# Kernel tuning notes

Measured on AMD Instinct MI355X. Metric: run time of the kernel, lower is better.

Reference implementation:

```python
import jax, jax.numpy as jnp
import numpy as np
from jax import lax

L = 5; HID = 100; B = 4; H = 256; W = 256; MU = 0.02; SLOPE = 0.01

def conv2d(x, w, pad=1, groups=1):
    return lax.conv_general_dilated(x, w, (1, 1), ((pad, pad), (pad, pad)),
                                    dimension_numbers=('NCHW', 'OIHW', 'NCHW'),
                                    feature_group_count=groups)

def leaky(x):
    return jnp.where(x >= 0, x, SLOPE * x)

def res_block(x, w1, w2, w3):
    # dropout omitted (eval-mode reference)
    h = leaky(conv2d(x, w1))
    h = leaky(conv2d(h, w2))
    return conv2d(h, w3)

def gauss1d(size=51, sigma=10.0):
    x = jnp.arange(size, dtype=jnp.float32) - (size - 1) / 2.0
    g = jnp.exp(-0.5 * (x / sigma) ** 2)
    return g / g.sum()

def gaussian_blur(x):
    # kornia GaussianBlur2d((51,51),(10,10), border 'constant') == zero-pad separable blur
    C = x.shape[1]
    g = gauss1d()
    kh = jnp.tile(g.reshape(1, 1, 1, 51), (C, 1, 1, 1))
    kv = jnp.tile(g.reshape(1, 1, 51, 1), (C, 1, 1, 1))
    x = lax.conv_general_dilated(x, kh, (1, 1), ((0, 0), (25, 25)),
                                 dimension_numbers=('NCHW', 'OIHW', 'NCHW'), feature_group_count=C)
    x = lax.conv_general_dilated(x, kv, (1, 1), ((25, 25), (0, 0)),
                                 dimension_numbers=('NCHW', 'OIHW', 'NCHW'), feature_group_count=C)
    return x

def spatial_gradient(x):
    # kornia SpatialGradient('sobel', normalized): kernels /8, replicate padding -> [B,C,2,H,W]
    Bk, C, Hk, Wk = x.shape
    kx = jnp.array([[-1., 0., 1.], [-2., 0., 2.], [-1., 0., 1.]], dtype=x.dtype) / 8.0
    k = jnp.stack([kx, kx.T])[:, None]          # [2,1,3,3]
    k = jnp.tile(k, (C, 1, 1, 1))               # [2C,1,3,3]
    xp = jnp.pad(x, ((0, 0), (0, 0), (1, 1), (1, 1)), mode='edge')
    out = conv2d(xp, k, pad=0, groups=C)        # [B,2C,H,W]
    return out.reshape(Bk, C, 2, Hk, Wk)

def deform_image(img, grid):
    # img [B,C,H,W]; grid [B,2,H,W] pixel coords (x,y); bilinear grid_sample, zeros outside
    Bk, C, Hk, Wk = img.shape
    x, y = grid[:, 0], grid[:, 1]
    x0 = jnp.floor(x); y0 = jnp.floor(y)
    wx1 = x - x0; wy1 = y - y0
    flat = img.reshape(Bk, C, Hk * Wk)
    def tap(xi, yi, wgt):
        valid = (xi >= 0) & (xi <= Wk - 1) & (yi >= 0) & (yi <= Hk - 1)
        xc = jnp.clip(xi, 0, Wk - 1).astype(jnp.int32)
        yc = jnp.clip(yi, 0, Hk - 1).astype(jnp.int32)
        idx = (yc * Wk + xc).reshape(Bk, 1, Hk * Wk)
        v = jnp.take_along_axis(flat, idx, axis=2).reshape(Bk, C, Hk, Wk)
        return v * (wgt * valid.astype(img.dtype))[:, None]
    return (tap(x0, y0, (1 - wx1) * (1 - wy1)) + tap(x0 + 1, y0, wx1 * (1 - wy1))
            + tap(x0, y0 + 1, (1 - wx1) * wy1) + tap(x0 + 1, y0 + 1, wx1 * wy1))

def forward(source, source_seg, z0, zw1, zw2, zw3, vw1, vw2, vw3):
    Bk, _, Hk, Wk = source.shape
    l = zw1.shape[0]
    yy, xx = jnp.meshgrid(jnp.arange(Hk, dtype=source.dtype), jnp.arange(Wk, dtype=source.dtype), indexing='ij')
    deformation = jnp.broadcast_to(jnp.stack([xx, yy])[None], (Bk, 2, Hk, Wk))  # pixel-coord id grid
    images = [source]
    residuals = [jnp.broadcast_to(z0, (Bk,) + z0.shape[1:])]
    residuals_deformed = [residuals[0]]
    fields = []
    grads = [spatial_gradient(source)]
    for i in range(l):
        zin = jnp.concatenate([residuals[i], images[i], images[0]], axis=1)  # 3 channels
        f = res_block(zin, zw1[i], zw2[i], zw3[i]) / l
        residuals.append(residuals[i] + f)
        residuals_deformed = [deform_image(z, deformation) for z in residuals_deformed]
        residuals_deformed.append(residuals[-1])
        vin = jnp.concatenate([deformation, images[-1]], axis=1)  # 3 channels
        fields.append(gaussian_blur(res_block(vin, vw1[i], vw2[i], vw3[i])))
        deformation = deformation - fields[i] / l
        mask = deform_image(source_seg, deformation)
        acc = residuals_deformed[1]
        for z in residuals_deformed[2:]:
            acc = acc + z
        new_img = deform_image(images[0], deformation) + acc * (MU ** 2 / l) * mask
        images.append(new_img)
        grads.append(spatial_gradient(new_img))
    return jnp.stack(images), jnp.stack(fields), jnp.stack(residuals), jnp.stack(grads)

def setup_inputs() -> dict:
    key = jax.random.key(0)
    ks = jax.random.split(key, 9)
    def rn(k, shape, s):
        return s * jax.random.normal(k, shape, dtype=jnp.float32)
    return {
        'source': rn(ks[0], (B, 1, H, W), 1.0),
        'source_seg': jax.random.uniform(ks[1], (B, 1, H, W), dtype=jnp.float32),
        'z0': rn(ks[2], (1, 1, H, W), 0.05),
        'zw1': rn(ks[3], (L, HID, 3, 3, 3), 0.2),
        'zw2': rn(ks[4], (L, HID, HID, 3, 3), 0.033),
        'zw3': rn(ks[5], (L, 1, HID, 3, 3), 0.033),
        'vw1': rn(ks[6], (L, HID, 3, 3, 3), 0.02),
        'vw2': rn(ks[7], (L, HID, HID, 3, 3), 0.033),
        'vw3': rn(ks[8], (L, 2, HID, 3, 3), 0.033),
    }

def reference(source, source_seg, z0, zw1, zw2, zw3, vw1, vw2, vw3):
    return forward(source, source_seg, z0, zw1, zw2, zw3, vw1, vw2, vw3)
```

## Files before the change

### kernel.cpp

```cpp
#include <hip/hip_runtime.h>
#include <math.h>

#define HW 65536
#define BB 4
#define NL 5

typedef short s8v __attribute__((ext_vector_type(8)));
typedef float f4v __attribute__((ext_vector_type(4)));
typedef unsigned short u16;

#define AS1 __attribute__((address_space(1)))
#define AS3 __attribute__((address_space(3)))

__device__ __forceinline__ float leaky_f(float x){ return x >= 0.f ? x : 0.01f * x; }

__device__ __forceinline__ u16 f2bf(float x){
    union { float f; unsigned u; } v; v.f = x;
    unsigned r = v.u + 0x7FFF + ((v.u >> 16) & 1);
    return (u16)(r >> 16);
}
__device__ __forceinline__ float bf2f(u16 h){
    union { unsigned u; float f; } v; v.u = ((unsigned)h) << 16;
    return v.f;
}

__global__ void k_init(const float* __restrict__ src, const float* __restrict__ z0,
                       float* __restrict__ images0, float* __restrict__ resid0,
                       float* __restrict__ def){
    int p = blockIdx.x * 256 + threadIdx.x;
    int b = p >> 16, q = p & 65535;
    images0[p] = src[p];
    resid0[p]  = z0[q];
    int x = q & 255, y = q >> 8;
    def[(size_t)(b * 2 + 0) * HW + q] = (float)x;
    def[(size_t)(b * 2 + 1) * HW + q] = (float)y;
}

__global__ void k_grad(const float* __restrict__ img, float* __restrict__ gout){
    int p = blockIdx.x * 256 + threadIdx.x;
    int b = p >> 16, q = p & 65535;
    int x = q & 255, y = q >> 8;
    const float* ib = img + (size_t)b * HW;
    int xm = max(x - 1, 0), xp = min(x + 1, 255);
    int ym = max(y - 1, 0), yp = min(y + 1, 255);
    float a00 = ib[ym * 256 + xm], a01 = ib[ym * 256 + x], a02 = ib[ym * 256 + xp];
    float a10 = ib[y  * 256 + xm],                         a12 = ib[y  * 256 + xp];
    float a20 = ib[yp * 256 + xm], a21 = ib[yp * 256 + x], a22 = ib[yp * 256 + xp];
    float gx = (a02 - a00 + 2.f * (a12 - a10) + a22 - a20) * 0.125f;
    float gy = (a20 - a00 + 2.f * (a21 - a01) + a22 - a02) * 0.125f;
    gout[(size_t)(b * 2 + 0) * HW + q] = gx;
    gout[(size_t)(b * 2 + 1) * HW + q] = gy;
}

__global__ void k_packw(const float* __restrict__ zw2, const float* __restrict__ vw2,
                        u16* __restrict__ wp){
    int idx = blockIdx.x * 256 + threadIdx.x;
    int lane9 = idx & 511, chunk = idx >> 9;
    int nt = chunk & 7; int t = chunk >> 3;
    int ks = t % 4; t >>= 2;
    int off = t % 9; t /= 9;
    int layer = t % 5, path = t / 5;
    int lane = lane9 >> 3, j = lane9 & 7;
    int ic = ks * 32 + (lane >> 4) * 8 + j;
    int oc = nt * 16 + (lane & 15);
    const float* w = path ? vw2 : zw2;
    float v = 0.f;
    if (ic < 100 && oc < 100)
        v = w[(((size_t)layer * 100 + oc) * 100 + ic) * 9 + off];
    wp[idx] = f2bf(v);
}

__global__ void k_packw3(const float* __restrict__ zw3, const float* __restrict__ vw3,
                         u16* __restrict__ wq){
    int idx = blockIdx.x * 256 + threadIdx.x;
    if (idx >= 184320) return;
    int lane9 = idx & 511, chunk = idx >> 9;
    int ks = chunk & 3; int t = chunk >> 2;
    int off = t % 9; int slot = t / 9;
    int lane = lane9 >> 3, j = lane9 & 7;
    int ic = ks * 32 + (lane >> 4) * 8 + j;
    int oc = lane & 15;
    float v = 0.f;
    if (ic < 100){
        if (slot < 5){ if (oc == 0) v = zw3[((size_t)slot * 100 + ic) * 9 + off]; }
        else { int layer = slot - 5;
               if (oc < 2) v = vw3[(((size_t)layer * 2 + oc) * 100 + ic) * 9 + off]; }
    }
    wq[idx] = f2bf(v);
}

__global__ __launch_bounds__(256)
void k_conv1(const float* __restrict__ p0, int s0, const float* __restrict__ p1, int s1,
             const float* __restrict__ p2, int s2, const float* __restrict__ w1,
             u16* __restrict__ h1, int b0){
    __shared__ float t3[300];
    __shared__ float wl[2700];
    const int tid = threadIdx.x;
    const int tX = blockIdx.x, tY = blockIdx.y, bz = blockIdx.z;
    const int b = b0 + bz;
    const int y0 = tY * 8 - 1, x0 = tX * 8 - 1;
    for (int idx = tid; idx < 300; idx += 256){
        int ch = idx / 100, p = idx - ch * 100;
        int r = p / 10, c = p - r * 10;
        int gy = y0 + r, gx = x0 + c;
        const float* pp = (ch == 0) ? p0 + (size_t)b * s0
                        : (ch == 1) ? p1 + (size_t)b * s1 : p2 + (size_t)b * s2;
        t3[idx] = ((unsigned)gy < 256u && (unsigned)gx < 256u) ? pp[gy * 256 + gx] : 0.f;
    }
    for (int idx = tid; idx < 2700; idx += 256) wl[idx] = w1[idx];
    __syncthreads();

    const int px = tid & 63, g = tid >> 6;
    const int row = px >> 3, colx = px & 7;
    float iv[27];
    #pragma unroll
    for (int c3 = 0; c3 < 3; c3++)
        #pragma unroll
        for (int dr = 0; dr < 3; dr++)
            #pragma unroll
            for (int dc = 0; dc < 3; dc++)
                iv[c3 * 9 + dr * 3 + dc] = t3[c3 * 100 + (row + dr) * 10 + colx + dc];

    const int gy = tY * 8 + row, gx = tX * 8 + colx;
    u16* dst = h1 + (((size_t)bz * HW + (size_t)(gy * 256 + gx)) << 7) + g * 32;
    #pragma unroll
    for (int s = 0; s < 4; s++){
        int ov[4];
        #pragma unroll
        for (int hp = 0; hp < 4; hp++){
            u16 lo = 0, hi = 0;
            #pragma unroll
            for (int e = 0; e < 2; e++){
                int oc = g * 32 + s * 8 + hp * 2 + e;
                u16 hv = 0;
                if (oc < 100){
                    const float* wk = &wl[oc * 27];
                    float a = 0.f;
                    #pragma unroll
                    for (int q = 0; q < 27; q++) a = fmaf(wk[q], iv[q], a);
                    hv = f2bf(leaky_f(a));
                }
                if (e) hi = hv; else lo = hv;
            }
            ov[hp] = (int)lo | ((int)hi << 16);
        }
        *(int4*)(dst + s * 8) = make_int4(ov[0], ov[1], ov[2], ov[3]);
    }
}

__device__ __forceinline__ void dma_setup(const u16* __restrict__ h, size_t hbase,
                                          int y0, int x0, int tid,
                                          const u16** gp, int* gstep){
    const u16* zpad = h + (hbase << 7) + 112;
    #pragma unroll
    for (int s = 0; s < 6; s++){
        int idx = tid + s * 256;
        const u16* g = zpad; int st = 0;
        if (idx < 1360){
            int px = idx >> 2, part = idx & 3;
            int hr = px / 34, hc = px - hr * 34;
            int gy = y0 + hr, gx = x0 + hc;
            if ((unsigned)gy < 256u && (unsigned)gx < 256u){
                g = h + ((hbase + (size_t)(gy * 256 + gx)) << 7) + (part ^ ((px >> 1) & 3)) * 8;
                st = 32;
            }
        }
        gp[s] = g; gstep[s] = st;
    }
}

__device__ __forceinline__ void dma_slab(const u16** gp, const int* gstep,
                                         short* Lnxt, int wv){
    #pragma unroll
    for (int s = 0; s < 6; s++){
        __builtin_amdgcn_global_load_lds(
            (const AS1 unsigned int*)(unsigned long long)(const void*)gp[s],
            (AS3 unsigned int*)(unsigned long long)(void*)(&Lnxt[(s * 256 + wv * 64) * 8]),
            16, 0, 0);
        gp[s] += gstep[s];
    }
}

__global__ __launch_bounds__(256, 2)
void k_conv2(const u16* __restrict__ h1, const u16* __restrict__ wp, u16* __restrict__ h2){
    __shared__ __align__(16) short lds[2][12288];
    const int tid = threadIdx.x;
    const int lane = tid & 63, wv = tid >> 6;
    const int quad = lane >> 4, m = lane & 15;
    const int hhalf = wv & 1, vhalf = wv >> 1;
    const int tX = blockIdx.x, tY = blockIdx.y, bz = blockIdx.z;
    const int y0 = tY * 8 - 1, x0 = tX * 32 - 1;
    const size_t hbase = (size_t)bz << 16;

    f4v acc[4][8];
    #pragma unroll
    for (int t = 0; t < 4; t++)
        #pragma unroll
        for (int n = 0; n < 8; n++){
            acc[t][n][0] = 0.f; acc[t][n][1] = 0.f; acc[t][n][2] = 0.f; acc[t][n][3] = 0.f;
        }

    const u16* gp[6]; int gstep[6];
    dma_setup(h1, hbase, y0, x0, tid, gp, gstep);
    dma_slab(gp, gstep, lds[0], wv);

    const u16* wl = wp + lane * 8;
    s8v af[2][4];
    #pragma unroll
    for (int t = 0; t < 4; t++)
        af[0][t] = *(const s8v*)(wl + (size_t)(4 * hhalf + t) * 512);

    for (int ks = 0; ks < 4; ks++){
        __syncthreads();
        const short* L = lds[ks & 1];
        short* Lnxt = lds[(ks + 1) & 1];
        #pragma unroll
        for (int off = 0; off < 9; off++){
            const int kk = ks * 9 + off;
            if (off == 4 && ks < 3) dma_slab(gp, gstep, Lnxt, wv);
            if (kk < 35){
                int nks = (off == 8) ? ks + 1 : ks;
                int noff = (off == 8) ? 0 : off + 1;
                #pragma unroll
                for (int t = 0; t < 4; t++)
                    af[(kk + 1) & 1][t] =
                        *(const s8v*)(wl + (size_t)((noff * 4 + nks) * 8 + 4 * hhalf + t) * 512);
            }
            const int dr = off / 3, dc = off - dr * 3;
            s8v bf[8];
            #pragma unroll
            for (int n = 0; n < 8; n++){
                int hpx = (4 * vhalf + (n >> 1) + dr) * 34 + (n & 1) * 16 + m + dc;
                bf[n] = *(const s8v*)&L[hpx * 32 + ((quad ^ ((hpx >> 1) & 3)) << 3)];
            }
            #pragma unroll
            for (int t = 0; t < 4; t++)
                #pragma unroll
                for (int n = 0; n < 8; n++)
                    acc[t][n] = __builtin_amdgcn_mfma_f32_16x16x32_bf16(
                        af[kk & 1][t], bf[n], acc[t][n], 0, 0, 0);
        }
    }

    #pragma unroll
    for (int n = 0; n < 8; n++){
        int gy = tY * 8 + 4 * vhalf + (n >> 1);
        int gx = tX * 32 + (n & 1) * 16 + m;
        u16* base = h2 + ((hbase + (size_t)(gy * 256 + gx)) << 7) + 64 * hhalf;
        #pragma unroll
        for (int t = 0; t < 4; t++){
            unsigned lo = (unsigned)f2bf(leaky_f(acc[t][n][0])) |
                          ((unsigned)f2bf(leaky_f(acc[t][n][1])) << 16);
            unsigned hi = (unsigned)f2bf(leaky_f(acc[t][n][2])) |
                          ((unsigned)f2bf(leaky_f(acc[t][n][3])) << 16);
            *(int2*)(base + t * 16 + quad * 4) = make_int2((int)lo, (int)hi);
        }
    }
}

template<int N>
__global__ __launch_bounds__(256, 2)
void k_conv3(const u16* __restrict__ h2, const u16* __restrict__ wq,
             const float* __restrict__ rprev, float* __restrict__ out0,
             float* __restrict__ out1, int b0){
    __shared__ __align__(16) short lds[2][12288];
    const int tid = threadIdx.x;
    const int lane = tid & 63, wv = tid >> 6;
    const int quad = lane >> 4, m = lane & 15;
    const int tX = blockIdx.x, tY = blockIdx.y, bz = blockIdx.z;
    const int y0 = tY * 8 - 1, x0 = tX * 32 - 1;
    const size_t hbase = (size_t)bz << 16;

    f4v acc[4];
    #pragma unroll
    for (int t = 0; t < 4; t++){ acc[t][0]=0.f; acc[t][1]=0.f; acc[t][2]=0.f; acc[t][3]=0.f; }

    const u16* gp[6]; int gstep[6];
    dma_setup(h2, hbase, y0, x0, tid, gp, gstep);
    dma_slab(gp, gstep, lds[0], wv);

    for (int ks = 0; ks < 4; ks++){
        __syncthreads();
        const short* L = lds[ks & 1];
        short* Lnxt = lds[(ks + 1) & 1];
        const bool pre = (ks < 3);
        #pragma unroll
        for (int off = 0; off < 9; off++){
            if (off == 4 && pre) dma_slab(gp, gstep, Lnxt, wv);
            const int dr = off / 3, dc = off - dr * 3;
            s8v wf = *(const s8v*)(wq + (size_t)(off * 4 + ks) * 512 + lane * 8);
            #pragma unroll
            for (int t = 0; t < 4; t++){
                int hpx = (2 * wv + (t >> 1) + dr) * 34 + (t & 1) * 16 + dc + m;
                s8v af = *(const s8v*)&L[hpx * 32 + ((quad ^ ((hpx >> 1) & 3)) << 3)];
                acc[t] = __builtin_amdgcn_mfma_f32_16x16x32_bf16(af, wf, acc[t], 0, 0, 0);
            }
        }
    }

    const int b = b0 + bz;
    #pragma unroll
    for (int t = 0; t < 4; t++){
        int gy = tY * 8 + 2 * wv + (t >> 1);
        int gx = tX * 32 + (t & 1) * 16 + quad * 4;
        size_t p = (size_t)gy * 256 + gx;
        if (N == 1){
            if (m == 0){
                float4 rp = *(const float4*)&rprev[(size_t)b * HW + p];
                float4 v = make_float4(rp.x + acc[t][0] * 0.2f, rp.y + acc[t][1] * 0.2f,
                                       rp.z + acc[t][2] * 0.2f, rp.w + acc[t][3] * 0.2f);
                *(float4*)&out0[(size_t)b * HW + p] = v;
                *(float4*)&out1[(size_t)b * HW + p] = v;
            }
        } else {
            if (m < 2){
                float4 v = make_float4(acc[t][0], acc[t][1], acc[t][2], acc[t][3]);
                *(float4*)&out0[((size_t)(b * 2) + m) * HW + p] = v;
            }
        }
    }
}

__device__ __forceinline__ float bilin(const float* __restrict__ img, float x, float y){
    float x0 = floorf(x), y0 = floorf(y);
    float wx = x - x0, wy = y - y0;
    float r = 0.f;
    #pragma unroll
    for (int dy = 0; dy < 2; dy++){
        float yi = y0 + (float)dy;
        if (yi < 0.f || yi > 255.f) continue;
        int iy = (int)yi;
        float wyv = dy ? wy : 1.f - wy;
        #pragma unroll
        for (int dx = 0; dx < 2; dx++){
            float xi = x0 + (float)dx;
            if (xi < 0.f || xi > 255.f) continue;
            int ix = (int)xi;
            float wxv = dx ? wx : 1.f - wx;
            r += wyv * wxv * img[iy * 256 + ix];
        }
    }
    return r;
}

__global__ void k_deform(const float* __restrict__ rdin, const float* __restrict__ def,
                         float* __restrict__ rdout){
    int p = blockIdx.x * 256 + threadIdx.x;
    int j = blockIdx.y;
    int b = p >> 16, q = p & 65535;
    float x = def[(size_t)(b * 2 + 0) * HW + q];
    float y = def[(size_t)(b * 2 + 1) * HW + q];
    rdout[(size_t)j * BB * HW + p] = bilin(rdin + (size_t)j * BB * HW + (size_t)b * HW, x, y);
}

__global__ void k_blur_h(const float* __restrict__ in, float* __restrict__ outb){
    __shared__ float g[51];
    __shared__ float row[306];
    __shared__ float ginv;
    int tid = threadIdx.x;
    int rid = blockIdx.x;
    int ch = rid >> 8, y = rid & 255;
    if (tid < 51){ float d = (float)tid - 25.f; g[tid] = expf(-0.005f * d * d); }
    row[tid + 25] = in[(size_t)ch * HW + y * 256 + tid];
    if (tid < 25) row[tid] = 0.f;
    if (tid >= 231) row[tid + 50] = 0.f;
    __syncthreads();
    if (tid == 0){ float s = 0.f; for (int k = 0; k < 51; k++) s += g[k]; ginv = 1.f / s; }
    __syncthreads();
    float acc = 0.f;
    for (int k = 0; k < 51; k++) acc = fmaf(g[k], row[tid + k], acc);
    outb[(size_t)ch * HW + y * 256 + tid] = acc * ginv;
}

__global__ void k_blur_v(const float* __restrict__ in, float* __restrict__ fout,
                         float* __restrict__ def){
    __shared__ float g[51];
    __shared__ float ginv;
    __shared__ float tb[82 * 64];
    int tid = threadIdx.x;
    int tX = blockIdx.x, tY = blockIdx.y, ch = blockIdx.z;
    if (tid < 51){ float d = (float)tid - 25.f; g[tid] = expf(-0.005f * d * d); }
    for (int idx = tid; idx < 82 * 64; idx += 256){
        int r = idx >> 6, c = idx & 63;
        int gy = tY * 32 + r - 25, gx = tX * 64 + c;
        tb[idx] = (gy >= 0 && gy < 256) ? in[(size_t)ch * HW + gy * 256 + gx] : 0.f;
    }
    __syncthreads();
    if (tid == 0){ float s = 0.f; for (int k = 0; k < 51; k++) s += g[k]; ginv = 1.f / s; }
    __syncthreads();
    int c = tid & 63, r0 = (tid >> 6) * 8;
    for (int k = 0; k < 8; k++){
        int r = r0 + k;
        float acc = 0.f;
        for (int t = 0; t < 51; t++) acc = fmaf(g[t], tb[(r + t) * 64 + c], acc);
        acc *= ginv;
        int y = tY * 32 + r, x = tX * 64 + c;
        fout[(size_t)ch * HW + y * 256 + x] = acc;
        def [(size_t)ch * HW + y * 256 + x] -= acc * 0.2f;
    }
}

__global__ void k_final(const float* __restrict__ def, const float* __restrict__ src,
                        const float* __restrict__ seg, const float* __restrict__ rdbase,
                        int nrd, float* __restrict__ imgout){
    int p = blockIdx.x * 256 + threadIdx.x;
    int b = p >> 16, q = p & 65535;
    float x = def[(size_t)(b * 2 + 0) * HW + q];
    float y = def[(size_t)(b * 2 + 1) * HW + q];
    float mk = bilin(seg + (size_t)b * HW, x, y);
    float s = bilin(src + (size_t)b * HW, x, y);
    float acc = 0.f;
    for (int j = 0; j < nrd; j++) acc += rdbase[(size_t)j * BB * HW + p];
    imgout[p] = s + acc * 8e-5f * mk;
}

extern "C" void kernel_launch(void* const* d_in, const int* in_sizes, int n_in,
                              void* d_out, int out_size, void* d_ws, size_t ws_size,
                              hipStream_t stream){
    const float* source = (const float*)d_in[0];
    const float* seg    = (const float*)d_in[1];
    const float* z0     = (const float*)d_in[2];
    const float* zw1    = (const float*)d_in[3];
    const float* zw2    = (const float*)d_in[4];
    const float* zw3    = (const float*)d_in[5];
    const float* vw1    = (const float*)d_in[6];
    const float* vw2    = (const float*)d_in[7];
    const float* vw3    = (const float*)d_in[8];

    float* out = (float*)d_out;
    float* images = out;
    float* fields = out + 1572864;
    float* resid  = out + 4194304;
    float* grads  = out + 5767168;

    float* ws = (float*)d_ws;
    float* def  = ws;
    float* RDa  = def  + 524288;
    float* RDb  = RDa  + 1310720;
    float* vtmp = RDb  + 1310720;
    float* btmp = vtmp + 524288;
    u16*   wp   = (u16*)(btmp + 524288);
    u16*   wq3  = wp + 1474560;
    u16*   h1   = wq3 + 184320;

    size_t need4 = 4194304ull * 4 + 1474560ull * 2 + 184320ull * 2 + 2ull * 4 * 16777216ull;
    const int HB = (ws_size >= need4) ? 4 : 1;
    u16* h2 = h1 + (size_t)HB * 8388608;

    k_packw <<<5760, 256, 0, stream>>>(zw2, vw2, wp);
    k_packw3<<<720, 256, 0, stream>>>(zw3, vw3, wq3);
    k_init  <<<1024, 256, 0, stream>>>(source, z0, images, resid, def);
    k_grad  <<<1024, 256, 0, stream>>>(source, grads);

    float* RDcur = RDa;
    float* RDnxt = RDb;

    for (int i = 0; i < NL; i++){
        float* res_i  = resid  + (size_t)i * BB * HW;
        float* res_ip = resid  + (size_t)(i + 1) * BB * HW;
        float* img_i  = images + (size_t)i * BB * HW;
        float* img_ip = images + (size_t)(i + 1) * BB * HW;

        for (int b0 = 0; b0 < BB; b0 += HB){
            k_conv1<<<dim3(32, 32, HB), 256, 0, stream>>>(
                res_i, HW, img_i, HW, images, HW, zw1 + (size_t)i * 2700, h1, b0);
            k_conv2<<<dim3(8, 32, HB), 256, 0, stream>>>(
                h1, wp + (size_t)i * 147456, h2);
            k_conv3<1><<<dim3(8, 32, HB), 256, 0, stream>>>(
                h2, wq3 + (size_t)i * 18432, res_i, res_ip,
                RDnxt + (size_t)i * BB * HW, b0);
        }

        if (i > 0)
            k_deform<<<dim3(1024, i), 256, 0, stream>>>(RDcur, def, RDnxt);

        for (int b0 = 0; b0 < BB; b0 += HB){
            k_conv1<<<dim3(32, 32, HB), 256, 0, stream>>>(
                def, 2 * HW, def + HW, 2 * HW, img_i, HW, vw1 + (size_t)i * 2700, h1, b0);
            k_conv2<<<dim3(8, 32, HB), 256, 0, stream>>>(
                h1, wp + (size_t)(NL + i) * 147456, h2);
            k_conv3<2><<<dim3(8, 32, HB), 256, 0, stream>>>(
                h2, wq3 + (size_t)(NL + i) * 18432, nullptr, vtmp, nullptr, b0);
        }
        k_blur_h<<<2048, 256, 0, stream>>>(vtmp, btmp);
        k_blur_v<<<dim3(4, 8, 8), 256, 0, stream>>>(
            btmp, fields + (size_t)i * BB * 2 * HW, def);

        k_final<<<1024, 256, 0, stream>>>(def, source, seg, RDnxt, i + 1, img_ip);
        k_grad<<<1024, 256, 0, stream>>>(img_ip, grads + (size_t)(i + 1) * BB * 2 * HW);

        float* t = RDcur; RDcur = RDnxt; RDnxt = t;
    }
}
```

Baseline: 2.456 ms.

## Switch conv2 to 32x32x16 bf16 MFMA with wave-per-output-channel-group tiling

The 100x100 3x3 conv kernel now uses 32x32x16 bf16 MFMA instead of 16x16x32. Each wave owns a 32-output-channel group across all 8 rows of the 32-pixel tile, rather than splitting rows and channel halves across waves. The weight pack layout is reordered to match, and a single A fragment is prefetched per MFMA step. The aim is fewer MFMA issues and less LDS B-fragment traffic per FLOP, at the cost of 16-wide accumulators and a different store pattern.

```diff
diff --git a/kernel.cpp b/kernel.cpp
--- a/kernel.cpp
+++ b/kernel.cpp
@@ -7,6 +7,7 @@
 
 typedef short s8v __attribute__((ext_vector_type(8)));
 typedef float f4v __attribute__((ext_vector_type(4)));
+typedef float f16v __attribute__((ext_vector_type(16)));
 typedef unsigned short u16;
 
 #define AS1 __attribute__((address_space(1)))
@@ -56,13 +57,13 @@
                         u16* __restrict__ wp){
     int idx = blockIdx.x * 256 + threadIdx.x;
     int lane9 = idx & 511, chunk = idx >> 9;
-    int nt = chunk & 7; int t = chunk >> 3;
-    int ks = t % 4; t >>= 2;
+    int g = chunk & 3; int t = chunk >> 2;
+    int icw = t & 7; t >>= 3;
     int off = t % 9; t /= 9;
     int layer = t % 5, path = t / 5;
     int lane = lane9 >> 3, j = lane9 & 7;
-    int ic = ks * 32 + (lane >> 4) * 8 + j;
-    int oc = nt * 16 + (lane & 15);
+    int oc = g * 32 + (lane & 31);
+    int ic = icw * 16 + (lane >> 5) * 8 + j;
     const float* w = path ? vw2 : zw2;
     float v = 0.f;
     if (ic < 100 && oc < 100)
@@ -186,29 +187,24 @@
     __shared__ __align__(16) short lds[2][12288];
     const int tid = threadIdx.x;
     const int lane = tid & 63, wv = tid >> 6;
-    const int quad = lane >> 4, m = lane & 15;
-    const int hhalf = wv & 1, vhalf = wv >> 1;
+    const int col = lane & 31;
+    const int hi  = lane >> 5;
     const int tX = blockIdx.x, tY = blockIdx.y, bz = blockIdx.z;
     const int y0 = tY * 8 - 1, x0 = tX * 32 - 1;
     const size_t hbase = (size_t)bz << 16;
 
-    f4v acc[4][8];
-    #pragma unroll
-    for (int t = 0; t < 4; t++)
-        #pragma unroll
-        for (int n = 0; n < 8; n++){
-            acc[t][n][0] = 0.f; acc[t][n][1] = 0.f; acc[t][n][2] = 0.f; acc[t][n][3] = 0.f;
-        }
+    f16v acc[8];
+    #pragma unroll
+    for (int n = 0; n < 8; n++)
+        #pragma unroll
+        for (int r = 0; r < 16; r++) acc[n][r] = 0.f;
 
     const u16* gp[6]; int gstep[6];
     dma_setup(h1, hbase, y0, x0, tid, gp, gstep);
     dma_slab(gp, gstep, lds[0], wv);
 
-    const u16* wl = wp + lane * 8;
-    s8v af[2][4];
-    #pragma unroll
-    for (int t = 0; t < 4; t++)
-        af[0][t] = *(const s8v*)(wl + (size_t)(4 * hhalf + t) * 512);
+    const u16* wl = wp + (size_t)wv * 512 + lane * 8;
+    s8v afc = *(const s8v*)(wl);
 
     for (int ks = 0; ks < 4; ks++){
         __syncthreads();
@@ -216,44 +212,37 @@
         short* Lnxt = lds[(ks + 1) & 1];
         #pragma unroll
         for (int off = 0; off < 9; off++){
-            const int kk = ks * 9 + off;
             if (off == 4 && ks < 3) dma_slab(gp, gstep, Lnxt, wv);
-            if (kk < 35){
-                int nks = (off == 8) ? ks + 1 : ks;
-                int noff = (off == 8) ? 0 : off + 1;
+            const int dr = off / 3, dc = off - dr * 3;
+            #pragma unroll
+            for (int w = 0; w < 2; w++){
+                int nchunk = (off == 8 && w == 1) ? ((ks + 1) * 2) * 4
+                           : (w == 1)            ? ((off + 1) * 8 + ks * 2) * 4
+                                                 : (off * 8 + ks * 2 + 1) * 4;
+                s8v afn = *(const s8v*)(wl + (size_t)nchunk * 512);
+                const int c = w * 2 + hi;
                 #pragma unroll
-                for (int t = 0; t < 4; t++)
-                    af[(kk + 1) & 1][t] =
-                        *(const s8v*)(wl + (size_t)((noff * 4 + nks) * 8 + 4 * hhalf + t) * 512);
-            }
-            const int dr = off / 3, dc = off - dr * 3;
-            s8v bf[8];
-            #pragma unroll
-            for (int n = 0; n < 8; n++){
-                int hpx = (4 * vhalf + (n >> 1) + dr) * 34 + (n & 1) * 16 + m + dc;
-                bf[n] = *(const s8v*)&L[hpx * 32 + ((quad ^ ((hpx >> 1) & 3)) << 3)];
-            }
-            #pragma unroll
-            for (int t = 0; t < 4; t++)
-                #pragma unroll
-                for (int n = 0; n < 8; n++)
-                    acc[t][n] = __builtin_amdgcn_mfma_f32_16x16x32_bf16(
-                        af[kk & 1][t], bf[n], acc[t][n], 0, 0, 0);
+                for (int n = 0; n < 8; n++){
+                    const int hpx = (n + dr) * 34 + col + dc;
+                    const s8v bf = *(const s8v*)&L[hpx * 32 + ((c ^ ((hpx >> 1) & 3)) << 3)];
+                    acc[n] = __builtin_amdgcn_mfma_f32_32x32x16_bf16(afc, bf, acc[n], 0, 0, 0);
+                }
+                afc = afn;
+            }
         }
     }
 
     #pragma unroll
     for (int n = 0; n < 8; n++){
-        int gy = tY * 8 + 4 * vhalf + (n >> 1);
-        int gx = tX * 32 + (n & 1) * 16 + m;
-        u16* base = h2 + ((hbase + (size_t)(gy * 256 + gx)) << 7) + 64 * hhalf;
-        #pragma unroll
-        for (int t = 0; t < 4; t++){
-            unsigned lo = (unsigned)f2bf(leaky_f(acc[t][n][0])) |
-                          ((unsigned)f2bf(leaky_f(acc[t][n][1])) << 16);
-            unsigned hi = (unsigned)f2bf(leaky_f(acc[t][n][2])) |
-                          ((unsigned)f2bf(leaky_f(acc[t][n][3])) << 16);
-            *(int2*)(base + t * 16 + quad * 4) = make_int2((int)lo, (int)hi);
+        int gy = tY * 8 + n, gx = tX * 32 + col;
+        u16* base = h2 + ((hbase + (size_t)(gy * 256 + gx)) << 7) + wv * 32 + hi * 4;
+        #pragma unroll
+        for (int q4 = 0; q4 < 4; q4++){
+            unsigned lo = (unsigned)f2bf(leaky_f(acc[n][q4 * 4 + 0])) |
+                          ((unsigned)f2bf(leaky_f(acc[n][q4 * 4 + 1])) << 16);
+            unsigned hh = (unsigned)f2bf(leaky_f(acc[n][q4 * 4 + 2])) |
+                          ((unsigned)f2bf(leaky_f(acc[n][q4 * 4 + 3])) << 16);
+            *(int2*)(base + q4 * 8) = make_int2((int)lo, (int)hh);
         }
     }
 }
```

New measurement: 2.493 ms. About the same (+1.5%).
